# Kernel tuning notes

Measured on AMD Instinct MI355X. Metric: run time of the kernel, lower is better.

The kernel has to match this reference:

```python
import jax, jax.numpy as jnp
import numpy as np

B, S, H, M, T = 64, 512, 768, 512, 26


def setup_inputs() -> dict:
    key = jax.random.key(0)
    ks = jax.random.split(key, 10)
    hidden = jax.random.normal(ks[0], (B, S, H), dtype=jnp.float32)
    W1 = jax.random.normal(ks[1], (M, H), dtype=jnp.float32) * 0.02
    b1 = jnp.zeros((M,), jnp.float32)
    W2 = jax.random.normal(ks[2], (T, M), dtype=jnp.float32) * 0.02
    b2 = jnp.zeros((T,), jnp.float32)
    start_trans = jax.random.normal(ks[3], (T,), dtype=jnp.float32) * 0.1
    end_trans = jax.random.normal(ks[4], (T,), dtype=jnp.float32) * 0.1
    trans = jax.random.normal(ks[5], (T, T), dtype=jnp.float32) * 0.1
    labels = jax.random.randint(ks[6], (B, S), 0, T, dtype=jnp.int32)
    lengths = jax.random.randint(ks[7], (B,), 1, S + 1, dtype=jnp.int32)
    return dict(hidden=hidden, W1=W1, b1=b1, W2=W2, b2=b2,
                start_trans=start_trans, end_trans=end_trans, trans=trans,
                labels=labels, lengths=lengths)


def _crf_nll(emissions, labels, lengths, start_trans, end_trans, trans):
    # emissions: [B,S,T]; labels: [B,S]; lengths: [B]
    maskf = (jnp.arange(S)[None, :] < lengths[:, None]).astype(emissions.dtype)  # [B,S]

    # --- numerator: score of the gold path (torchcrf _compute_score) ---
    emit_gold = jnp.take_along_axis(emissions, labels[..., None], axis=-1)[..., 0]  # [B,S]
    trans_gold = trans[labels[:, :-1], labels[:, 1:]]  # [B,S-1]
    last_tags = jnp.take_along_axis(labels, (lengths - 1)[:, None], axis=1)[:, 0]  # [B]
    numerator = (start_trans[labels[:, 0]] + emit_gold[:, 0]
                 + jnp.sum((trans_gold + emit_gold[:, 1:]) * maskf[:, 1:], axis=1)
                 + end_trans[last_tags])  # [B]

    # --- denominator: log partition via forward algorithm (lax.scan) ---
    alpha0 = start_trans[None, :] + emissions[:, 0]  # [B,T]
    emis_t = jnp.swapaxes(emissions[:, 1:], 0, 1)    # [S-1,B,T]
    mask_t = jnp.swapaxes(maskf[:, 1:] > 0, 0, 1)    # [S-1,B] bool

    def step(alpha, xs):
        emit, m = xs
        # alpha[b,i] + trans[i,j] + emit[b,j] -> logsumexp over i
        nxt = jax.nn.logsumexp(alpha[:, :, None] + trans[None, :, :] + emit[:, None, :], axis=1)
        return jnp.where(m[:, None], nxt, alpha), None

    alpha, _ = jax.lax.scan(step, alpha0, (emis_t, mask_t))
    denominator = jax.nn.logsumexp(alpha + end_trans[None, :], axis=1)  # [B]

    llh = numerator - denominator
    return -jnp.mean(llh)  # loss = -crf(..., reduction='mean')


def reference(hidden, W1, b1, W2, b2, start_trans, end_trans, trans, labels, lengths):
    h = jnp.einsum('bsh,mh->bsm', hidden, W1) + b1      # fc1 (no activation in source)
    emissions = jnp.einsum('bsm,tm->bst', h, W2) + b2   # fc2 -> [B,S,T]
    return _crf_nll(emissions, labels, lengths, start_trans, end_trans, trans)
```

## Files before the change

kernel.cpp:

```cpp
#include <hip/hip_runtime.h>
#include <math.h>

#define Bn 64
#define Sn 512
#define Hn 768
#define Mn 512
#define Tn 26
#define TP 32

#define OFF_BC    0
#define OFF_BFRAG 32
#define OFF_EX    (32 + 12288)
#define EXSZ      ((size_t)Bn*Sn*TP)
#define OFF_QG    (OFF_EX + EXSZ)
#define QGSZ      524288
#define OFF_ACC   (OFF_QG + QGSZ)
#define OFF_CNT   (OFF_ACC + 1)

typedef __attribute__((ext_vector_type(8)))  short bfrag;
typedef __attribute__((ext_vector_type(4)))  float f32x4;
typedef __attribute__((ext_vector_type(16))) float f32x16;

__device__ __forceinline__ short f2bf(float f) {
    unsigned u = __float_as_uint(f);
    unsigned r = (u + 0x7FFFu + ((u >> 16) & 1u)) >> 16;
    return (short)r;
}
__device__ __forceinline__ unsigned cvtpk(float a, float b) {
    unsigned r;
    asm("v_cvt_pk_bf16_f32 %0, %1, %2" : "=v"(r) : "v"(a), "v"(b));
    return r;
}
__device__ __forceinline__ void pswap(unsigned &a, unsigned &b) {
    asm("v_permlane32_swap_b32 %0, %1" : "+v"(a), "+v"(b));
}
__device__ __forceinline__ bfrag mkfrag(unsigned a, unsigned b, unsigned c, unsigned d) {
    union { unsigned u[4]; bfrag v; } x;
    x.u[0] = a; x.u[1] = b; x.u[2] = c; x.u[3] = d;
    return x.v;
}
__device__ __forceinline__ float rl(float x, int i) {
    return __uint_as_float(__builtin_amdgcn_readlane(__float_as_uint(x), i));
}

__global__ __launch_bounds__(256) void k_prep(const float* __restrict__ W1,
                                              const float* __restrict__ b1,
                                              const float* __restrict__ W2,
                                              const float* __restrict__ b2,
                                              float* __restrict__ ws) {
    const int bx = blockIdx.x;
    const int tid = threadIdx.x;
    if (bx == 48) {
        if (tid == 0) {
            ws[OFF_ACC] = 0.f;
            ((unsigned*)ws)[OFF_CNT] = 0u;
        }
        if (tid < TP) {
            float bcv = 0.f;
            if (tid < Tn) {
                float a0 = 0.f, a1 = 0.f, a2 = 0.f, a3 = 0.f;
                const float4* w2 = reinterpret_cast<const float4*>(W2 + (size_t)tid * Mn);
                const float4* bb = reinterpret_cast<const float4*>(b1);
                for (int m = 0; m < Mn / 4; ++m) {
                    float4 w = w2[m], v = bb[m];
                    a0 = fmaf(w.x, v.x, a0); a1 = fmaf(w.y, v.y, a1);
                    a2 = fmaf(w.z, v.z, a2); a3 = fmaf(w.w, v.w, a3);
                }
                bcv = b2[tid] + (a0 + a1) + (a2 + a3);
            }
            ws[OFF_BC + tid] = bcv;
        }
        return;
    }

    __shared__ float mrg[3][64][8];
    const int lane = tid & 63;
    const int wv   = tid >> 6;
    const int k0   = bx * 16;
    const int colA = lane & 15;
    const int mj   = ((lane >> 4) & 3) * 8;

    f32x4 acc0 = {0.f, 0.f, 0.f, 0.f}, acc1 = {0.f, 0.f, 0.f, 0.f};
    for (int mq = 0; mq < 4; ++mq) {
        const int m0 = wv * 128 + mq * 32;
        bfrag av, bv0, bv1;
#pragma unroll
        for (int j = 0; j < 8; ++j)
            av[j] = f2bf(W1[(size_t)(m0 + mj + j) * Hn + k0 + colA]);
        {
            const float* p = W2 + (size_t)(lane & 15) * Mn + m0 + mj;
            float4 x = *reinterpret_cast<const float4*>(p);
            float4 y = *reinterpret_cast<const float4*>(p + 4);
            bv0 = mkfrag(cvtpk(x.x, x.y), cvtpk(x.z, x.w), cvtpk(y.x, y.y), cvtpk(y.z, y.w));
        }
        {
            int c = 16 + (lane & 15);
            bfrag z = {};
            if (c < Tn) {
                const float* p = W2 + (size_t)c * Mn + m0 + mj;
                float4 x = *reinterpret_cast<const float4*>(p);
                float4 y = *reinterpret_cast<const float4*>(p + 4);
                z = mkfrag(cvtpk(x.x, x.y), cvtpk(x.z, x.w), cvtpk(y.x, y.y), cvtpk(y.z, y.w));
            }
            bv1 = z;
        }
        acc0 = __builtin_amdgcn_mfma_f32_16x16x32_bf16(av, bv0, acc0, 0, 0, 0);
        acc1 = __builtin_amdgcn_mfma_f32_16x16x32_bf16(av, bv1, acc1, 0, 0, 0);
    }

    if (wv > 0) {
#pragma unroll
        for (int i = 0; i < 4; ++i) {
            mrg[wv - 1][lane][i]     = acc0[i];
            mrg[wv - 1][lane][4 + i] = acc1[i];
        }
    }
    __syncthreads();
    if (wv == 0) {
        unsigned short* Bfo = (unsigned short*)(ws + OFF_BFRAG);
#pragma unroll
        for (int i = 0; i < 4; ++i) {
            float v0 = acc0[i] + mrg[0][lane][i]     + mrg[1][lane][i]     + mrg[2][lane][i];
            float v1 = acc1[i] + mrg[0][lane][4 + i] + mrg[1][lane][4 + i] + mrg[2][lane][4 + i];
            int k   = k0 + ((lane >> 4) & 3) * 4 + i;
            int ks2 = k >> 5;
            int fl  = ((k >> 3) & 3) * 16 + (lane & 15);
            Bfo[((size_t)(ks2 * 2 + 0) * 64 + fl) * 8 + (k & 7)] = (unsigned short)f2bf(v0);
            Bfo[((size_t)(ks2 * 2 + 1) * 64 + fl) * 8 + (k & 7)] = (unsigned short)f2bf(v1);
        }
    }
}

#define LOADK(KS, FA, FB, BV0, BV1)                                                        \
    {                                                                                      \
        const float* ap = abase + (KS) * 32;                                               \
        FA = *reinterpret_cast<const float4*>(ap);                                         \
        FB = *reinterpret_cast<const float4*>(ap + 4);                                     \
        BV0 = *reinterpret_cast<const bfrag*>(Bf + ((size_t)((KS) * 2 + 0) * 64 + l) * 8); \
        BV1 = *reinterpret_cast<const bfrag*>(Bf + ((size_t)((KS) * 2 + 1) * 64 + l) * 8); \
    }

__global__ __launch_bounds__(64, 2) void k_gemm(const float* __restrict__ hidden,
                                                const float* __restrict__ ws,
                                                float* __restrict__ Eexp) {
    const int l    = threadIdx.x;
    const int row0 = blockIdx.x * 16;
    const int arow = row0 + (l & 15);
    const int kg   = l >> 4;
    const float* abase = hidden + (size_t)arow * Hn + kg * 8;
    const unsigned short* Bf = (const unsigned short*)(ws + OFF_BFRAG);

    f32x4 acc0 = {0.f, 0.f, 0.f, 0.f}, acc1 = {0.f, 0.f, 0.f, 0.f};

    float4 fa0, fb0, fa1, fb1;
    bfrag bv00, bv01, bv10, bv11;
    LOADK(0, fa0, fb0, bv00, bv01);
    LOADK(1, fa1, fb1, bv10, bv11);

#pragma unroll 1
    for (int ks = 0; ks < 22; ks += 2) {
        float4 ta, tb; bfrag t0, t1;
        LOADK(ks + 2, ta, tb, t0, t1);
        bfrag av = mkfrag(cvtpk(fa0.x, fa0.y), cvtpk(fa0.z, fa0.w),
                          cvtpk(fb0.x, fb0.y), cvtpk(fb0.z, fb0.w));
        acc0 = __builtin_amdgcn_mfma_f32_16x16x32_bf16(av, bv00, acc0, 0, 0, 0);
        acc1 = __builtin_amdgcn_mfma_f32_16x16x32_bf16(av, bv01, acc1, 0, 0, 0);
        fa0 = ta; fb0 = tb; bv00 = t0; bv01 = t1;

        float4 ua, ub; bfrag u0, u1;
        LOADK(ks + 3, ua, ub, u0, u1);
        av = mkfrag(cvtpk(fa1.x, fa1.y), cvtpk(fa1.z, fa1.w),
                    cvtpk(fb1.x, fb1.y), cvtpk(fb1.z, fb1.w));
        acc0 = __builtin_amdgcn_mfma_f32_16x16x32_bf16(av, bv10, acc0, 0, 0, 0);
        acc1 = __builtin_amdgcn_mfma_f32_16x16x32_bf16(av, bv11, acc1, 0, 0, 0);
        fa1 = ua; fb1 = ub; bv10 = u0; bv11 = u1;
    }
    {
        bfrag av = mkfrag(cvtpk(fa0.x, fa0.y), cvtpk(fa0.z, fa0.w),
                          cvtpk(fb0.x, fb0.y), cvtpk(fb0.z, fb0.w));
        acc0 = __builtin_amdgcn_mfma_f32_16x16x32_bf16(av, bv00, acc0, 0, 0, 0);
        acc1 = __builtin_amdgcn_mfma_f32_16x16x32_bf16(av, bv01, acc1, 0, 0, 0);
        av = mkfrag(cvtpk(fa1.x, fa1.y), cvtpk(fa1.z, fa1.w),
                    cvtpk(fb1.x, fb1.y), cvtpk(fb1.z, fb1.w));
        acc0 = __builtin_amdgcn_mfma_f32_16x16x32_bf16(av, bv10, acc0, 0, 0, 0);
        acc1 = __builtin_amdgcn_mfma_f32_16x16x32_bf16(av, bv11, acc1, 0, 0, 0);
    }

    const int c0 = l & 15;
    const int rbase = row0 + kg * 4;
    float bc0 = ws[OFF_BC + c0], bc1 = ws[OFF_BC + 16 + c0];
#pragma unroll
    for (int i = 0; i < 4; ++i) {
        Eexp[(size_t)(rbase + i) * TP + c0]      = __expf(acc0[i] + bc0);
        Eexp[(size_t)(rbase + i) * TP + 16 + c0] = __expf(acc1[i] + bc1);
    }
}

__global__ __launch_bounds__(256) void k_chunk(const float* __restrict__ Eexp,
                                               const float* __restrict__ trans,
                                               const int* __restrict__ lengths,
                                               unsigned* __restrict__ Qg) {
    __shared__ float Ech[4][32][32];
    const int tid  = threadIdx.x;
    const int wv   = tid >> 6;
    const int lane = tid & 63;
    const int task = blockIdx.x * 4 + wv;
    const int b    = task >> 4;
    const int c    = task & 15;
    const int len  = lengths[b];
    const int s0   = c * 32;
    int nact = len - 1 - s0;
    nact = nact < 0 ? 0 : (nact > 32 ? 32 : nact);
    const int t = lane & 31;
    const int h = lane >> 5;

    {
        const float* Eb = Eexp + (size_t)b * Sn * TP;
        int lr = lane >> 1, hf = lane & 1;
        int s = s0 + 1 + lr; s = s > 511 ? 511 : s;
        const float4* src = reinterpret_cast<const float4*>(Eb + (size_t)s * TP + hf * 16);
        float4* dst = reinterpret_cast<float4*>(&Ech[wv][lr][hf * 16]);
        dst[0] = src[0]; dst[1] = src[1]; dst[2] = src[2]; dst[3] = src[3];
    }

    bfrag A0, A1, B0, B1;
#pragma unroll
    for (int j = 0; j < 8; ++j) {
        int k0 = 8 * h + j, k1 = 16 + 8 * h + j;
        A0[j] = (t < Tn && k0 < Tn) ? f2bf(__expf(trans[k0 * Tn + t]) * 0.03125f) : (short)0;
        A1[j] = (t < Tn && k1 < Tn) ? f2bf(__expf(trans[k1 * Tn + t]) * 0.03125f) : (short)0;
        B0[j] = (k0 == t) ? (short)0x3F80 : (short)0;
        B1[j] = (k1 == t) ? (short)0x3F80 : (short)0;
    }

    float qf[16];
#pragma unroll
    for (int r = 0; r < 16; ++r) {
        int row = (r & 3) + 8 * (r >> 2) + 4 * h;
        qf[r] = (row == t) ? 1.f : 0.f;
    }

    for (int j = 0; j < nact; ++j) {
        f32x16 acc = {};
        acc = __builtin_amdgcn_mfma_f32_32x32x16_bf16(A0, B0, acc, 0, 0, 0);
        acc = __builtin_amdgcn_mfma_f32_32x32x16_bf16(A1, B1, acc, 0, 0, 0);
        const float* ep = &Ech[wv][j][4 * h];
        float4 e0 = *reinterpret_cast<const float4*>(ep);
        float4 e1 = *reinterpret_cast<const float4*>(ep + 8);
        float4 e2 = *reinterpret_cast<const float4*>(ep + 16);
        float4 e3 = *reinterpret_cast<const float4*>(ep + 24);
        float ev[16];
        ev[0]  = e0.x; ev[1]  = e0.y; ev[2]  = e0.z; ev[3]  = e0.w;
        ev[4]  = e1.x; ev[5]  = e1.y; ev[6]  = e1.z; ev[7]  = e1.w;
        ev[8]  = e2.x; ev[9]  = e2.y; ev[10] = e2.z; ev[11] = e2.w;
        ev[12] = e3.x; ev[13] = e3.y; ev[14] = e3.z; ev[15] = e3.w;
#pragma unroll
        for (int r = 0; r < 16; ++r) qf[r] = acc[r] * ev[r];
        if (j + 1 < nact) {
            unsigned W0 = cvtpk(qf[0],  qf[1]),  W1 = cvtpk(qf[2],  qf[3]);
            unsigned W2 = cvtpk(qf[4],  qf[5]),  W3 = cvtpk(qf[6],  qf[7]);
            unsigned W4 = cvtpk(qf[8],  qf[9]),  W5 = cvtpk(qf[10], qf[11]);
            unsigned W6 = cvtpk(qf[12], qf[13]), W7 = cvtpk(qf[14], qf[15]);
            pswap(W0, W2); pswap(W1, W3); pswap(W4, W6); pswap(W5, W7);
            B0 = mkfrag(W0, W1, W2, W3);
            B1 = mkfrag(W4, W5, W6, W7);
        }
    }

    unsigned* qdst = Qg + (size_t)task * 512;
#pragma unroll
    for (int g = 0; g < 4; ++g) {
        unsigned u0 = cvtpk(qf[4*g + 0], qf[4*g + 1]);
        unsigned u1 = cvtpk(qf[4*g + 2], qf[4*g + 3]);
        qdst[(4*g + 2*h)     * 32 + t] = u0;
        qdst[(4*g + 2*h + 1) * 32 + t] = u1;
    }
}

__global__ __launch_bounds__(128) void k_comb(const float* __restrict__ Eexp,
                                              const unsigned* __restrict__ Qg,
                                              const float* __restrict__ start_t,
                                              const float* __restrict__ end_t,
                                              const float* __restrict__ trans,
                                              const int* __restrict__ labels,
                                              const int* __restrict__ lengths,
                                              float* __restrict__ accp,
                                              unsigned* __restrict__ cntp,
                                              float* __restrict__ out) {
    const int tid  = threadIdx.x;
    const int b    = blockIdx.x;
    const int len  = lengths[b];
    const int wv   = tid >> 6;
    const int lane = tid & 63;

    if (wv == 0) {
        const int t = lane & 31;
        float alpha = (t < Tn) ? __expf(start_t[t]) * Eexp[(size_t)b * Sn * TP + t] : 0.f;
        float logZ = 0.f;
        const unsigned* Qb = Qg + (size_t)b * 16 * 512 + t;
        unsigned q0[16], q1[16];
#pragma unroll
        for (int p = 0; p < 16; ++p) q0[p] = Qb[p * 32];
        for (int c = 0; c < 16; ++c) {
            int cn = c < 15 ? c + 1 : 15;
#pragma unroll
            for (int p = 0; p < 16; ++p) q1[p] = Qb[(size_t)cn * 512 + p * 32];
            float p0 = 0.f, p1 = 0.f, p2 = 0.f, p3 = 0.f;
#pragma unroll
            for (int p = 0; p < 16; p += 2) {
                unsigned ua = q0[p];
                unsigned ub = q0[p + 1];
                p0 = fmaf(rl(alpha, 2*p    ), __uint_as_float(ua << 16),          p0);
                p1 = fmaf(rl(alpha, 2*p + 1), __uint_as_float(ua & 0xFFFF0000u), p1);
                p2 = fmaf(rl(alpha, 2*p + 2), __uint_as_float(ub << 16),          p2);
                p3 = fmaf(rl(alpha, 2*p + 3), __uint_as_float(ub & 0xFFFF0000u), p3);
            }
            float v = (p0 + p1) + (p2 + p3);
            float C = __uint_as_float(__builtin_amdgcn_readfirstlane(__float_as_uint(v)));
            alpha = v / C;
            logZ += __logf(C);
#pragma unroll
            for (int p = 0; p < 16; ++p) q0[p] = q1[p];
        }
        float dv = (t < Tn && lane < 32) ? alpha * __expf(end_t[t]) : 0.f;
#pragma unroll
        for (int off = 32; off; off >>= 1) dv += __shfl_xor(dv, off);
        if (lane == 0) {
            float denom = logZ + __logf(dv) + (float)(len - 1) * 3.46573590279973f;
            atomicAdd(accp, -denom);
            __threadfence();
            unsigned old = atomicAdd(cntp, 1u);
            if (old == 2u * Bn - 1u) {
                float tot = atomicAdd(accp, 0.0f);
                out[0] = -tot * (1.0f / 64.0f);
            }
        }
    } else {
        const int base = b * Sn;
        const float* Eb2 = Eexp + (size_t)base * TP;
        float part = 0.f;
        for (int s2 = 1 + lane; s2 < len; s2 += 64) {
            int lp = labels[base + s2 - 1];
            int lc = labels[base + s2];
            part += trans[lp * Tn + lc] + __logf(Eb2[(size_t)s2 * TP + lc]);
        }
#pragma unroll
        for (int off = 32; off; off >>= 1) part += __shfl_xor(part, off);
        if (lane == 0) {
            int l0 = labels[base], ll = labels[base + len - 1];
            float numer = part + start_t[l0] + __logf(Eb2[l0]) + end_t[ll];
            atomicAdd(accp, numer);
            __threadfence();
            unsigned old = atomicAdd(cntp, 1u);
            if (old == 2u * Bn - 1u) {
                float tot = atomicAdd(accp, 0.0f);
                out[0] = -tot * (1.0f / 64.0f);
            }
        }
    }
}

extern "C" void kernel_launch(void* const* d_in, const int* in_sizes, int n_in,
                              void* d_out, int out_size, void* d_ws, size_t ws_size,
                              hipStream_t stream) {
    const float* hidden  = (const float*)d_in[0];
    const float* W1      = (const float*)d_in[1];
    const float* b1      = (const float*)d_in[2];
    const float* W2      = (const float*)d_in[3];
    const float* b2      = (const float*)d_in[4];
    const float* start_t = (const float*)d_in[5];
    const float* end_t   = (const float*)d_in[6];
    const float* trans   = (const float*)d_in[7];
    const int*   labels  = (const int*)d_in[8];
    const int*   lengths = (const int*)d_in[9];
    float* ws  = (float*)d_ws;
    float* out = (float*)d_out;

    hipLaunchKernelGGL(k_prep, dim3(49), dim3(256), 0, stream, W1, b1, W2, b2, ws);
    hipLaunchKernelGGL(k_gemm, dim3(2048), dim3(64), 0, stream, hidden, ws, ws + OFF_EX);
    hipLaunchKernelGGL(k_chunk, dim3(256), dim3(256), 0, stream, ws + OFF_EX, trans, lengths,
                       (unsigned*)(ws + OFF_QG));
    hipLaunchKernelGGL(k_comb, dim3(64), dim3(128), 0, stream, ws + OFF_EX,
                       (const unsigned*)(ws + OFF_QG), start_t, end_t, trans, labels,
                       lengths, ws + OFF_ACC, (unsigned*)(ws + OFF_CNT), out);
}
```

Before: 53.39 us.

## Fuse GEMM, chunk scan and combine into one kernel with per-batch counters

Merges the emission GEMM, the per-chunk transfer-matrix products and the final combine into a single kernel of 1024 blocks. Each block computes 32 emission rows for one (batch, chunk), keeps them in shared memory for the chunk scan, and the last block to finish for each batch (tracked by an atomic counter) runs the combine. This removes two kernel launches and the global round trip between the GEMM and the chunk stage. In exchange the GEMM grid shrinks from 2048 to 1024 blocks, only one wave per block runs the serial chunk scan, and correctness now relies on atomic counters and memory fences.

```diff
diff --git a/kernel.cpp b/kernel.cpp
--- a/kernel.cpp
+++ b/kernel.cpp
@@ -16,6 +16,7 @@
 #define QGSZ      524288
 #define OFF_ACC   (OFF_QG + QGSZ)
 #define OFF_CNT   (OFF_ACC + 1)
+#define OFF_CNTB  (OFF_CNT + 1)
 
 typedef __attribute__((ext_vector_type(8)))  short bfrag;
 typedef __attribute__((ext_vector_type(4)))  float f32x4;
@@ -55,6 +56,7 @@
             ws[OFF_ACC] = 0.f;
             ((unsigned*)ws)[OFF_CNT] = 0u;
         }
+        if (tid < 64) ((unsigned*)ws)[OFF_CNTB + tid] = 0u;
         if (tid < TP) {
             float bcv = 0.f;
             if (tid < Tn) {
@@ -140,169 +142,167 @@
         BV1 = *reinterpret_cast<const bfrag*>(Bf + ((size_t)((KS) * 2 + 1) * 64 + l) * 8); \
     }
 
-__global__ __launch_bounds__(64, 2) void k_gemm(const float* __restrict__ hidden,
-                                                const float* __restrict__ ws,
-                                                float* __restrict__ Eexp) {
-    const int l    = threadIdx.x;
-    const int row0 = blockIdx.x * 16;
-    const int arow = row0 + (l & 15);
-    const int kg   = l >> 4;
-    const float* abase = hidden + (size_t)arow * Hn + kg * 8;
-    const unsigned short* Bf = (const unsigned short*)(ws + OFF_BFRAG);
-
-    f32x4 acc0 = {0.f, 0.f, 0.f, 0.f}, acc1 = {0.f, 0.f, 0.f, 0.f};
-
-    float4 fa0, fb0, fa1, fb1;
-    bfrag bv00, bv01, bv10, bv11;
-    LOADK(0, fa0, fb0, bv00, bv01);
-    LOADK(1, fa1, fb1, bv10, bv11);
-
-#pragma unroll 1
-    for (int ks = 0; ks < 22; ks += 2) {
-        float4 ta, tb; bfrag t0, t1;
-        LOADK(ks + 2, ta, tb, t0, t1);
-        bfrag av = mkfrag(cvtpk(fa0.x, fa0.y), cvtpk(fa0.z, fa0.w),
-                          cvtpk(fb0.x, fb0.y), cvtpk(fb0.z, fb0.w));
-        acc0 = __builtin_amdgcn_mfma_f32_16x16x32_bf16(av, bv00, acc0, 0, 0, 0);
-        acc1 = __builtin_amdgcn_mfma_f32_16x16x32_bf16(av, bv01, acc1, 0, 0, 0);
-        fa0 = ta; fb0 = tb; bv00 = t0; bv01 = t1;
-
-        float4 ua, ub; bfrag u0, u1;
-        LOADK(ks + 3, ua, ub, u0, u1);
-        av = mkfrag(cvtpk(fa1.x, fa1.y), cvtpk(fa1.z, fa1.w),
-                    cvtpk(fb1.x, fb1.y), cvtpk(fb1.z, fb1.w));
-        acc0 = __builtin_amdgcn_mfma_f32_16x16x32_bf16(av, bv10, acc0, 0, 0, 0);
-        acc1 = __builtin_amdgcn_mfma_f32_16x16x32_bf16(av, bv11, acc1, 0, 0, 0);
-        fa1 = ua; fb1 = ub; bv10 = u0; bv11 = u1;
-    }
-    {
-        bfrag av = mkfrag(cvtpk(fa0.x, fa0.y), cvtpk(fa0.z, fa0.w),
-                          cvtpk(fb0.x, fb0.y), cvtpk(fb0.z, fb0.w));
-        acc0 = __builtin_amdgcn_mfma_f32_16x16x32_bf16(av, bv00, acc0, 0, 0, 0);
-        acc1 = __builtin_amdgcn_mfma_f32_16x16x32_bf16(av, bv01, acc1, 0, 0, 0);
-        av = mkfrag(cvtpk(fa1.x, fa1.y), cvtpk(fa1.z, fa1.w),
-                    cvtpk(fb1.x, fb1.y), cvtpk(fb1.z, fb1.w));
-        acc0 = __builtin_amdgcn_mfma_f32_16x16x32_bf16(av, bv10, acc0, 0, 0, 0);
-        acc1 = __builtin_amdgcn_mfma_f32_16x16x32_bf16(av, bv11, acc1, 0, 0, 0);
-    }
-
-    const int c0 = l & 15;
-    const int rbase = row0 + kg * 4;
-    float bc0 = ws[OFF_BC + c0], bc1 = ws[OFF_BC + 16 + c0];
-#pragma unroll
-    for (int i = 0; i < 4; ++i) {
-        Eexp[(size_t)(rbase + i) * TP + c0]      = __expf(acc0[i] + bc0);
-        Eexp[(size_t)(rbase + i) * TP + 16 + c0] = __expf(acc1[i] + bc1);
-    }
-}
-
-__global__ __launch_bounds__(256) void k_chunk(const float* __restrict__ Eexp,
-                                               const float* __restrict__ trans,
-                                               const int* __restrict__ lengths,
-                                               unsigned* __restrict__ Qg) {
-    __shared__ float Ech[4][32][32];
+__global__ __launch_bounds__(128, 2) void k_mega(const float* __restrict__ hidden,
+                                                 float* __restrict__ ws,
+                                                 const float* __restrict__ start_t,
+                                                 const float* __restrict__ end_t,
+                                                 const float* __restrict__ trans,
+                                                 const int* __restrict__ labels,
+                                                 const int* __restrict__ lengths,
+                                                 float* __restrict__ out) {
+    __shared__ float El[32][32];
+    __shared__ int isLast;
     const int tid  = threadIdx.x;
     const int wv   = tid >> 6;
-    const int lane = tid & 63;
-    const int task = blockIdx.x * 4 + wv;
-    const int b    = task >> 4;
-    const int c    = task & 15;
-    const int len  = lengths[b];
-    const int s0   = c * 32;
-    int nact = len - 1 - s0;
-    nact = nact < 0 ? 0 : (nact > 32 ? 32 : nact);
-    const int t = lane & 31;
-    const int h = lane >> 5;
+    const int l    = tid & 63;
+    const int bid  = blockIdx.x;
+    const int b    = bid >> 4;
+    const int c    = bid & 15;
+    const int kg   = l >> 4;
+    const int c0   = l & 15;
+    const unsigned short* Bf = (const unsigned short*)(ws + OFF_BFRAG);
+    float* Eexp = ws + OFF_EX;
+    unsigned* Qg = (unsigned*)(ws + OFF_QG);
+    float* accp = ws + OFF_ACC;
+    unsigned* cntp = (unsigned*)(ws + OFF_CNT);
+    unsigned* cntb = (unsigned*)(ws + OFF_CNTB);
 
     {
-        const float* Eb = Eexp + (size_t)b * Sn * TP;
-        int lr = lane >> 1, hf = lane & 1;
-        int s = s0 + 1 + lr; s = s > 511 ? 511 : s;
-        const float4* src = reinterpret_cast<const float4*>(Eb + (size_t)s * TP + hf * 16);
-        float4* dst = reinterpret_cast<float4*>(&Ech[wv][lr][hf * 16]);
-        dst[0] = src[0]; dst[1] = src[1]; dst[2] = src[2]; dst[3] = src[3];
-    }
-
-    bfrag A0, A1, B0, B1;
-#pragma unroll
-    for (int j = 0; j < 8; ++j) {
-        int k0 = 8 * h + j, k1 = 16 + 8 * h + j;
-        A0[j] = (t < Tn && k0 < Tn) ? f2bf(__expf(trans[k0 * Tn + t]) * 0.03125f) : (short)0;
-        A1[j] = (t < Tn && k1 < Tn) ? f2bf(__expf(trans[k1 * Tn + t]) * 0.03125f) : (short)0;
-        B0[j] = (k0 == t) ? (short)0x3F80 : (short)0;
-        B1[j] = (k1 == t) ? (short)0x3F80 : (short)0;
-    }
-
-    float qf[16];
-#pragma unroll
-    for (int r = 0; r < 16; ++r) {
-        int row = (r & 3) + 8 * (r >> 2) + 4 * h;
-        qf[r] = (row == t) ? 1.f : 0.f;
-    }
-
-    for (int j = 0; j < nact; ++j) {
-        f32x16 acc = {};
-        acc = __builtin_amdgcn_mfma_f32_32x32x16_bf16(A0, B0, acc, 0, 0, 0);
-        acc = __builtin_amdgcn_mfma_f32_32x32x16_bf16(A1, B1, acc, 0, 0, 0);
-        const float* ep = &Ech[wv][j][4 * h];
-        float4 e0 = *reinterpret_cast<const float4*>(ep);
-        float4 e1 = *reinterpret_cast<const float4*>(ep + 8);
-        float4 e2 = *reinterpret_cast<const float4*>(ep + 16);
-        float4 e3 = *reinterpret_cast<const float4*>(ep + 24);
-        float ev[16];
-        ev[0]  = e0.x; ev[1]  = e0.y; ev[2]  = e0.z; ev[3]  = e0.w;
-        ev[4]  = e1.x; ev[5]  = e1.y; ev[6]  = e1.z; ev[7]  = e1.w;
-        ev[8]  = e2.x; ev[9]  = e2.y; ev[10] = e2.z; ev[11] = e2.w;
-        ev[12] = e3.x; ev[13] = e3.y; ev[14] = e3.z; ev[15] = e3.w;
-#pragma unroll
-        for (int r = 0; r < 16; ++r) qf[r] = acc[r] * ev[r];
-        if (j + 1 < nact) {
-            unsigned W0 = cvtpk(qf[0],  qf[1]),  W1 = cvtpk(qf[2],  qf[3]);
-            unsigned W2 = cvtpk(qf[4],  qf[5]),  W3 = cvtpk(qf[6],  qf[7]);
-            unsigned W4 = cvtpk(qf[8],  qf[9]),  W5 = cvtpk(qf[10], qf[11]);
-            unsigned W6 = cvtpk(qf[12], qf[13]), W7 = cvtpk(qf[14], qf[15]);
-            pswap(W0, W2); pswap(W1, W3); pswap(W4, W6); pswap(W5, W7);
-            B0 = mkfrag(W0, W1, W2, W3);
-            B1 = mkfrag(W4, W5, W6, W7);
-        }
-    }
-
-    unsigned* qdst = Qg + (size_t)task * 512;
-#pragma unroll
-    for (int g = 0; g < 4; ++g) {
-        unsigned u0 = cvtpk(qf[4*g + 0], qf[4*g + 1]);
-        unsigned u1 = cvtpk(qf[4*g + 2], qf[4*g + 3]);
-        qdst[(4*g + 2*h)     * 32 + t] = u0;
-        qdst[(4*g + 2*h + 1) * 32 + t] = u1;
-    }
-}
-
-__global__ __launch_bounds__(128) void k_comb(const float* __restrict__ Eexp,
-                                              const unsigned* __restrict__ Qg,
-                                              const float* __restrict__ start_t,
-                                              const float* __restrict__ end_t,
-                                              const float* __restrict__ trans,
-                                              const int* __restrict__ labels,
-                                              const int* __restrict__ lengths,
-                                              float* __restrict__ accp,
-                                              unsigned* __restrict__ cntp,
-                                              float* __restrict__ out) {
-    const int tid  = threadIdx.x;
-    const int b    = blockIdx.x;
-    const int len  = lengths[b];
-    const int wv   = tid >> 6;
-    const int lane = tid & 63;
-
+        const int lr = wv * 16 + (l & 15);
+        const int s  = (c * 32 + 1 + lr) & 511;
+        const float* abase = hidden + ((size_t)b * Sn + s) * Hn + kg * 8;
+
+        f32x4 acc0 = {0.f, 0.f, 0.f, 0.f}, acc1 = {0.f, 0.f, 0.f, 0.f};
+        float4 fa0, fb0, fa1, fb1;
+        bfrag bv00, bv01, bv10, bv11;
+        LOADK(0, fa0, fb0, bv00, bv01);
+        LOADK(1, fa1, fb1, bv10, bv11);
+
+#pragma unroll 1
+        for (int ks = 0; ks < 22; ks += 2) {
+            float4 ta, tb; bfrag t0, t1;
+            LOADK(ks + 2, ta, tb, t0, t1);
+            bfrag av = mkfrag(cvtpk(fa0.x, fa0.y), cvtpk(fa0.z, fa0.w),
+                              cvtpk(fb0.x, fb0.y), cvtpk(fb0.z, fb0.w));
+            acc0 = __builtin_amdgcn_mfma_f32_16x16x32_bf16(av, bv00, acc0, 0, 0, 0);
+            acc1 = __builtin_amdgcn_mfma_f32_16x16x32_bf16(av, bv01, acc1, 0, 0, 0);
+            fa0 = ta; fb0 = tb; bv00 = t0; bv01 = t1;
+
+            float4 ua, ub; bfrag u0, u1;
+            LOADK(ks + 3, ua, ub, u0, u1);
+            av = mkfrag(cvtpk(fa1.x, fa1.y), cvtpk(fa1.z, fa1.w),
+                        cvtpk(fb1.x, fb1.y), cvtpk(fb1.z, fb1.w));
+            acc0 = __builtin_amdgcn_mfma_f32_16x16x32_bf16(av, bv10, acc0, 0, 0, 0);
+            acc1 = __builtin_amdgcn_mfma_f32_16x16x32_bf16(av, bv11, acc1, 0, 0, 0);
+            fa1 = ua; fb1 = ub; bv10 = u0; bv11 = u1;
+        }
+        {
+            bfrag av = mkfrag(cvtpk(fa0.x, fa0.y), cvtpk(fa0.z, fa0.w),
+                              cvtpk(fb0.x, fb0.y), cvtpk(fb0.z, fb0.w));
+            acc0 = __builtin_amdgcn_mfma_f32_16x16x32_bf16(av, bv00, acc0, 0, 0, 0);
+            acc1 = __builtin_amdgcn_mfma_f32_16x16x32_bf16(av, bv01, acc1, 0, 0, 0);
+            av = mkfrag(cvtpk(fa1.x, fa1.y), cvtpk(fa1.z, fa1.w),
+                        cvtpk(fb1.x, fb1.y), cvtpk(fb1.z, fb1.w));
+            acc0 = __builtin_amdgcn_mfma_f32_16x16x32_bf16(av, bv10, acc0, 0, 0, 0);
+            acc1 = __builtin_amdgcn_mfma_f32_16x16x32_bf16(av, bv11, acc1, 0, 0, 0);
+        }
+        const float bc0 = ws[OFF_BC + c0], bc1 = ws[OFF_BC + 16 + c0];
+        const int lrb = wv * 16 + kg * 4;
+#pragma unroll
+        for (int i = 0; i < 4; ++i) {
+            const int s2 = (c * 32 + 1 + lrb + i) & 511;
+            float e0 = __expf(acc0[i] + bc0);
+            float e1 = __expf(acc1[i] + bc1);
+            Eexp[((size_t)b * Sn + s2) * TP + c0]      = e0;
+            Eexp[((size_t)b * Sn + s2) * TP + 16 + c0] = e1;
+            El[lrb + i][c0]      = e0;
+            El[lrb + i][16 + c0] = e1;
+        }
+    }
+    __syncthreads();
+
+    const int len = lengths[b];
     if (wv == 0) {
-        const int t = lane & 31;
+        const int t = l & 31;
+        const int h = l >> 5;
+        const int s0 = c * 32;
+        int nact = len - 1 - s0;
+        nact = nact < 0 ? 0 : (nact > 32 ? 32 : nact);
+
+        bfrag A0, A1, B0, B1;
+#pragma unroll
+        for (int j = 0; j < 8; ++j) {
+            int k0 = 8 * h + j, k1 = 16 + 8 * h + j;
+            A0[j] = (t < Tn && k0 < Tn) ? f2bf(__expf(trans[k0 * Tn + t]) * 0.03125f) : (short)0;
+            A1[j] = (t < Tn && k1 < Tn) ? f2bf(__expf(trans[k1 * Tn + t]) * 0.03125f) : (short)0;
+            B0[j] = (k0 == t) ? (short)0x3F80 : (short)0;
+            B1[j] = (k1 == t) ? (short)0x3F80 : (short)0;
+        }
+
+        float qf[16];
+#pragma unroll
+        for (int r = 0; r < 16; ++r) {
+            int row = (r & 3) + 8 * (r >> 2) + 4 * h;
+            qf[r] = (row == t) ? 1.f : 0.f;
+        }
+
+        for (int j = 0; j < nact; ++j) {
+            f32x16 acc = {};
+            acc = __builtin_amdgcn_mfma_f32_32x32x16_bf16(A0, B0, acc, 0, 0, 0);
+            acc = __builtin_amdgcn_mfma_f32_32x32x16_bf16(A1, B1, acc, 0, 0, 0);
+            const float* ep = &El[j][4 * h];
+            float4 e0 = *reinterpret_cast<const float4*>(ep);
+            float4 e1 = *reinterpret_cast<const float4*>(ep + 8);
+            float4 e2 = *reinterpret_cast<const float4*>(ep + 16);
+            float4 e3 = *reinterpret_cast<const float4*>(ep + 24);
+            float ev[16];
+            ev[0]  = e0.x; ev[1]  = e0.y; ev[2]  = e0.z; ev[3]  = e0.w;
+            ev[4]  = e1.x; ev[5]  = e1.y; ev[6]  = e1.z; ev[7]  = e1.w;
+            ev[8]  = e2.x; ev[9]  = e2.y; ev[10] = e2.z; ev[11] = e2.w;
+            ev[12] = e3.x; ev[13] = e3.y; ev[14] = e3.z; ev[15] = e3.w;
+#pragma unroll
+            for (int r = 0; r < 16; ++r) qf[r] = acc[r] * ev[r];
+            if (j + 1 < nact) {
+                unsigned W0 = cvtpk(qf[0],  qf[1]),  W1 = cvtpk(qf[2],  qf[3]);
+                unsigned W2 = cvtpk(qf[4],  qf[5]),  W3 = cvtpk(qf[6],  qf[7]);
+                unsigned W4 = cvtpk(qf[8],  qf[9]),  W5 = cvtpk(qf[10], qf[11]);
+                unsigned W6 = cvtpk(qf[12], qf[13]), W7 = cvtpk(qf[14], qf[15]);
+                pswap(W0, W2); pswap(W1, W3); pswap(W4, W6); pswap(W5, W7);
+                B0 = mkfrag(W0, W1, W2, W3);
+                B1 = mkfrag(W4, W5, W6, W7);
+            }
+        }
+
+        unsigned* qdst = Qg + (size_t)bid * 512;
+#pragma unroll
+        for (int g = 0; g < 4; ++g) {
+            unsigned u0 = cvtpk(qf[4*g + 0], qf[4*g + 1]);
+            unsigned u1 = cvtpk(qf[4*g + 2], qf[4*g + 3]);
+            qdst[(4*g + 2*h)     * 32 + t] = u0;
+            qdst[(4*g + 2*h + 1) * 32 + t] = u1;
+        }
+    }
+    __syncthreads();
+
+    if (tid == 0) {
+        __threadfence();
+        unsigned old = atomicAdd(&cntb[b], 1u);
+        isLast = (old == 15u);
+    }
+    __syncthreads();
+    if (!isLast) return;
+    __threadfence();
+
+    if (wv == 0) {
+        const int t = l & 31;
         float alpha = (t < Tn) ? __expf(start_t[t]) * Eexp[(size_t)b * Sn * TP + t] : 0.f;
         float logZ = 0.f;
         const unsigned* Qb = Qg + (size_t)b * 16 * 512 + t;
         unsigned q0[16], q1[16];
 #pragma unroll
         for (int p = 0; p < 16; ++p) q0[p] = Qb[p * 32];
-        for (int c = 0; c < 16; ++c) {
-            int cn = c < 15 ? c + 1 : 15;
+        for (int cc = 0; cc < 16; ++cc) {
+            int cn = cc < 15 ? cc + 1 : 15;
 #pragma unroll
             for (int p = 0; p < 16; ++p) q1[p] = Qb[(size_t)cn * 512 + p * 32];
             float p0 = 0.f, p1 = 0.f, p2 = 0.f, p3 = 0.f;
@@ -322,10 +322,10 @@
 #pragma unroll
             for (int p = 0; p < 16; ++p) q0[p] = q1[p];
         }
-        float dv = (t < Tn && lane < 32) ? alpha * __expf(end_t[t]) : 0.f;
+        float dv = (t < Tn && l < 32) ? alpha * __expf(end_t[t]) : 0.f;
 #pragma unroll
         for (int off = 32; off; off >>= 1) dv += __shfl_xor(dv, off);
-        if (lane == 0) {
+        if (l == 0) {
             float denom = logZ + __logf(dv) + (float)(len - 1) * 3.46573590279973f;
             atomicAdd(accp, -denom);
             __threadfence();
@@ -339,14 +339,14 @@
         const int base = b * Sn;
         const float* Eb2 = Eexp + (size_t)base * TP;
         float part = 0.f;
-        for (int s2 = 1 + lane; s2 < len; s2 += 64) {
+        for (int s2 = 1 + l; s2 < len; s2 += 64) {
             int lp = labels[base + s2 - 1];
             int lc = labels[base + s2];
             part += trans[lp * Tn + lc] + __logf(Eb2[(size_t)s2 * TP + lc]);
         }
 #pragma unroll
         for (int off = 32; off; off >>= 1) part += __shfl_xor(part, off);
-        if (lane == 0) {
+        if (l == 0) {
             int l0 = labels[base], ll = labels[base + len - 1];
             float numer = part + start_t[l0] + __logf(Eb2[l0]) + end_t[ll];
             atomicAdd(accp, numer);
@@ -377,10 +377,6 @@
     float* out = (float*)d_out;
 
     hipLaunchKernelGGL(k_prep, dim3(49), dim3(256), 0, stream, W1, b1, W2, b2, ws);
-    hipLaunchKernelGGL(k_gemm, dim3(2048), dim3(64), 0, stream, hidden, ws, ws + OFF_EX);
-    hipLaunchKernelGGL(k_chunk, dim3(256), dim3(256), 0, stream, ws + OFF_EX, trans, lengths,
-                       (unsigned*)(ws + OFF_QG));
-    hipLaunchKernelGGL(k_comb, dim3(64), dim3(128), 0, stream, ws + OFF_EX,
-                       (const unsigned*)(ws + OFF_QG), start_t, end_t, trans, labels,
-                       lengths, ws + OFF_ACC, (unsigned*)(ws + OFF_CNT), out);
-}
+    hipLaunchKernelGGL(k_mega, dim3(1024), dim3(128), 0, stream, hidden, ws, start_t, end_t,
+                       trans, labels, lengths, out);
+}
```

After: 70.01 us. 1.31x slower.

## Fuse chunk and combine kernels using per-batch last-block atomic counter

Applied to the files above, without the earlier changes.

Merges the chunked transfer-matrix kernel and the per-sequence combine kernel into one launch. Each batch's four chunk blocks bump a per-batch counter after writing their partial products, and the last block to arrive runs the forward combine and the numerator for that sequence. This removes one kernel launch and the gap between launches, at the cost of atomics, fences and a serialized tail that runs in whichever block finishes last.

```diff
diff --git a/kernel.cpp b/kernel.cpp
--- a/kernel.cpp
+++ b/kernel.cpp
@@ -16,6 +16,7 @@
 #define QGSZ      524288
 #define OFF_ACC   (OFF_QG + QGSZ)
 #define OFF_CNT   (OFF_ACC + 1)
+#define OFF_CNTB  (OFF_CNT + 1)
 
 typedef __attribute__((ext_vector_type(8)))  short bfrag;
 typedef __attribute__((ext_vector_type(4)))  float f32x4;
@@ -55,6 +56,7 @@
             ws[OFF_ACC] = 0.f;
             ((unsigned*)ws)[OFF_CNT] = 0u;
         }
+        if (tid < 64) ((unsigned*)ws)[OFF_CNTB + tid] = 0u;
         if (tid < TP) {
             float bcv = 0.f;
             if (tid < Tn) {
@@ -196,16 +198,25 @@
     }
 }
 
-__global__ __launch_bounds__(256) void k_chunk(const float* __restrict__ Eexp,
+__global__ __launch_bounds__(256) void k_ccomb(const float* __restrict__ Eexp,
+                                               const float* __restrict__ start_t,
+                                               const float* __restrict__ end_t,
                                                const float* __restrict__ trans,
+                                               const int* __restrict__ labels,
                                                const int* __restrict__ lengths,
-                                               unsigned* __restrict__ Qg) {
+                                               unsigned* __restrict__ Qg,
+                                               float* __restrict__ accp,
+                                               unsigned* __restrict__ cntp,
+                                               unsigned* __restrict__ cntb,
+                                               float* __restrict__ out) {
     __shared__ float Ech[4][32][32];
+    __shared__ int isLast;
     const int tid  = threadIdx.x;
     const int wv   = tid >> 6;
     const int lane = tid & 63;
-    const int task = blockIdx.x * 4 + wv;
-    const int b    = task >> 4;
+    const int bid  = blockIdx.x;
+    const int task = bid * 4 + wv;
+    const int b    = bid >> 2;
     const int c    = task & 15;
     const int len  = lengths[b];
     const int s0   = c * 32;
@@ -267,42 +278,36 @@
         }
     }
 
-    unsigned* qdst = Qg + (size_t)task * 512;
-#pragma unroll
-    for (int g = 0; g < 4; ++g) {
-        unsigned u0 = cvtpk(qf[4*g + 0], qf[4*g + 1]);
-        unsigned u1 = cvtpk(qf[4*g + 2], qf[4*g + 3]);
-        qdst[(4*g + 2*h)     * 32 + t] = u0;
-        qdst[(4*g + 2*h + 1) * 32 + t] = u1;
-    }
-}
-
-__global__ __launch_bounds__(128) void k_comb(const float* __restrict__ Eexp,
-                                              const unsigned* __restrict__ Qg,
-                                              const float* __restrict__ start_t,
-                                              const float* __restrict__ end_t,
-                                              const float* __restrict__ trans,
-                                              const int* __restrict__ labels,
-                                              const int* __restrict__ lengths,
-                                              float* __restrict__ accp,
-                                              unsigned* __restrict__ cntp,
-                                              float* __restrict__ out) {
-    const int tid  = threadIdx.x;
-    const int b    = blockIdx.x;
-    const int len  = lengths[b];
-    const int wv   = tid >> 6;
-    const int lane = tid & 63;
+    {
+        unsigned* qdst = Qg + (size_t)task * 512;
+#pragma unroll
+        for (int g = 0; g < 4; ++g) {
+            unsigned u0 = cvtpk(qf[4*g + 0], qf[4*g + 1]);
+            unsigned u1 = cvtpk(qf[4*g + 2], qf[4*g + 3]);
+            qdst[(4*g + 2*h)     * 32 + t] = u0;
+            qdst[(4*g + 2*h + 1) * 32 + t] = u1;
+        }
+    }
+    __syncthreads();
+
+    if (tid == 0) {
+        __threadfence();
+        unsigned old = atomicAdd(&cntb[b], 1u);
+        isLast = (old == 3u);
+    }
+    __syncthreads();
+    if (!isLast) return;
+    __threadfence();
 
     if (wv == 0) {
-        const int t = lane & 31;
         float alpha = (t < Tn) ? __expf(start_t[t]) * Eexp[(size_t)b * Sn * TP + t] : 0.f;
         float logZ = 0.f;
         const unsigned* Qb = Qg + (size_t)b * 16 * 512 + t;
         unsigned q0[16], q1[16];
 #pragma unroll
         for (int p = 0; p < 16; ++p) q0[p] = Qb[p * 32];
-        for (int c = 0; c < 16; ++c) {
-            int cn = c < 15 ? c + 1 : 15;
+        for (int cc = 0; cc < 16; ++cc) {
+            int cn = cc < 15 ? cc + 1 : 15;
 #pragma unroll
             for (int p = 0; p < 16; ++p) q1[p] = Qb[(size_t)cn * 512 + p * 32];
             float p0 = 0.f, p1 = 0.f, p2 = 0.f, p3 = 0.f;
@@ -335,7 +340,7 @@
                 out[0] = -tot * (1.0f / 64.0f);
             }
         }
-    } else {
+    } else if (wv == 1) {
         const int base = b * Sn;
         const float* Eb2 = Eexp + (size_t)base * TP;
         float part = 0.f;
@@ -378,9 +383,8 @@
 
     hipLaunchKernelGGL(k_prep, dim3(49), dim3(256), 0, stream, W1, b1, W2, b2, ws);
     hipLaunchKernelGGL(k_gemm, dim3(2048), dim3(64), 0, stream, hidden, ws, ws + OFF_EX);
-    hipLaunchKernelGGL(k_chunk, dim3(256), dim3(256), 0, stream, ws + OFF_EX, trans, lengths,
-                       (unsigned*)(ws + OFF_QG));
-    hipLaunchKernelGGL(k_comb, dim3(64), dim3(128), 0, stream, ws + OFF_EX,
-                       (const unsigned*)(ws + OFF_QG), start_t, end_t, trans, labels,
-                       lengths, ws + OFF_ACC, (unsigned*)(ws + OFF_CNT), out);
-}
+    hipLaunchKernelGGL(k_ccomb, dim3(256), dim3(256), 0, stream, ws + OFF_EX, start_t,
+                       end_t, trans, labels, lengths, (unsigned*)(ws + OFF_QG),
+                       ws + OFF_ACC, (unsigned*)(ws + OFF_CNT),
+                       (unsigned*)(ws + OFF_CNTB), out);
+}
```

Result: slower. 77.20 us (+44.6%).
